# Kernel tuning notes

Hardware: AMD Instinct MI355X
Metric: run time of the kernel (lower is better)

## Reference

```python
import jax, jax.numpy as jnp
import numpy as np

EPS_N = 1e-12   # F.normalize eps
LN_EPS = 1e-5   # LayerNorm eps
N_NODES = 20000
NODES_PER_GRAPH = 200
DEG = 8
N_EDGES = N_NODES * DEG
F_NODE = 36
F_EDGE = 10
HID = 128
HEAD = 8
DK = HID // HEAD
G = N_NODES // NODES_PER_GRAPH


def l2norm(x):
    n = jnp.sqrt(jnp.sum(x * x, axis=-1, keepdims=True))
    return x / jnp.maximum(n, EPS_N)


def layer_norm(x, g, b):
    m = jnp.mean(x, axis=-1, keepdims=True)
    v = jnp.mean((x - m) ** 2, axis=-1, keepdims=True)
    return (x - m) / jnp.sqrt(v + LN_EPS) * g + b


def seg_softmax(e, idx, n):
    m = jax.ops.segment_max(e, idx, num_segments=n)
    ex = jnp.exp(e - m[idx])
    s = jax.ops.segment_sum(ex, idx, num_segments=n)
    return ex / s[idx]


def sfe_conv(x, src, dst, eattr, We, Wq, Wk, Wv, Wo, bo, g, b):
    # x: [N, in], src/dst: [Ef] (self loops included), eattr: [Ef, F_EDGE]
    n = x.shape[0]
    emb = l2norm(eattr @ We)                  # edge_encoder + F.normalize
    xj = x[src] + emb                          # source node + edge embedding
    q = (xj @ Wq).reshape(-1, HEAD, DK)
    ksum = (x[dst] @ Wk).reshape(-1, HEAD, DK).sum(axis=1)  # sum over k-heads (matmul+sum in source)
    v = (xj @ Wv).reshape(-1, HEAD, DK)
    energy = jnp.einsum('ehd,ed->eh', q, ksum) / jnp.sqrt(jnp.float32(HID))
    att = seg_softmax(energy, dst, n)          # segment softmax over target nodes, per head
    msg = (v * att[:, :, None]).reshape(-1, HID)
    agg = jax.ops.segment_sum(msg, dst, num_segments=n)
    y = layer_norm(agg @ Wo + bo, g, b)        # update(): out_norm(out_linear(.))
    return layer_norm(y, g, b)                 # forward() applies out_norm again


def setup_inputs():
    key = jax.random.key(0)
    ks = jax.random.split(key, 16)
    x = jax.random.normal(ks[0], (N_NODES, F_NODE), jnp.float32)
    edge_attr = jax.random.uniform(ks[1], (N_EDGES, F_EDGE), jnp.float32)
    src = jnp.repeat(jnp.arange(N_NODES), DEG)
    base = src - src % NODES_PER_GRAPH
    off = jax.random.randint(ks[2], (N_EDGES,), 1, NODES_PER_GRAPH)
    dst = base + (src % NODES_PER_GRAPH + off) % NODES_PER_GRAPH  # same-graph, no self loops
    edge_index = jnp.stack([src, dst]).astype(jnp.int64)
    batch = (jnp.arange(N_NODES) // NODES_PER_GRAPH).astype(jnp.int64)
    interface_pos = jnp.arange(0, N_NODES, 2, dtype=jnp.int64)
    s = lambda k, sh: jax.random.normal(k, sh, jnp.float32) * 0.05
    return dict(
        x=x, edge_attr=edge_attr,
        c0_We=s(ks[3], (F_EDGE, F_NODE)), c0_Wq=s(ks[4], (F_NODE, HID)),
        c0_Wk=s(ks[5], (F_NODE, HID)), c0_Wv=s(ks[6], (F_NODE, HID)),
        c0_Wo=s(ks[7], (HID, HID)), c0_bo=jnp.zeros((HID,), jnp.float32),
        c0_g=jnp.ones((HID,), jnp.float32), c0_b=jnp.zeros((HID,), jnp.float32),
        cs_We=s(ks[8], (2, F_EDGE, HID)), cs_Wq=s(ks[9], (2, HID, HID)),
        cs_Wk=s(ks[10], (2, HID, HID)), cs_Wv=s(ks[11], (2, HID, HID)),
        cs_Wo=s(ks[12], (2, HID, HID)), cs_bo=jnp.zeros((2, HID), jnp.float32),
        cs_g=jnp.ones((2, HID), jnp.float32), cs_b=jnp.zeros((2, HID), jnp.float32),
        gate=s(ks[13], (HID,)), W1=s(ks[14], (HID, HID // 2)),
        b1=jnp.zeros((HID // 2,), jnp.float32), W2=s(ks[15], (HID // 2, 1)),
        b2=jnp.zeros((1,), jnp.float32),
        edge_index=edge_index, batch=batch, interface_pos=interface_pos,
        graph_num=G)


def reference(x, edge_attr, c0_We, c0_Wq, c0_Wk, c0_Wv, c0_Wo, c0_bo, c0_g, c0_b,
              cs_We, cs_Wq, cs_Wk, cs_Wv, cs_Wo, cs_bo, cs_g, cs_b,
              gate, W1, b1, W2, b2, edge_index, batch, interface_pos, graph_num):
    n = x.shape[0]
    loops = jnp.arange(n)
    src = jnp.concatenate([edge_index[0], loops])
    dst = jnp.concatenate([edge_index[1], loops])
    ea = jnp.concatenate([l2norm(edge_attr),
                          jnp.zeros((n, edge_attr.shape[1]), edge_attr.dtype)])
    h = l2norm(x)
    h = jnp.tanh(sfe_conv(h, src, dst, ea, c0_We, c0_Wq, c0_Wk, c0_Wv, c0_Wo, c0_bo, c0_g, c0_b))
    for i in range(cs_We.shape[0]):
        h = jnp.tanh(sfe_conv(h, src, dst, ea, cs_We[i], cs_Wq[i], cs_Wk[i], cs_Wv[i],
                              cs_Wo[i], cs_bo[i], cs_g[i], cs_b[i]))
    # global self-attention pooling over interface nodes, per graph
    xi = h[interface_pos]
    bi = batch[interface_pos]
    att = seg_softmax(xi @ gate, bi, graph_num)
    pooled = jax.ops.segment_sum(att[:, None] * xi, bi, num_segments=graph_num)  # [G, HID]
    out = jnp.tanh(pooled @ W1 + b1)
    return jax.nn.sigmoid(out @ W2 + b2)  # [G, 1]
```

## Files before the change

### kernel.cpp

```cpp
#include <hip/hip_runtime.h>
#include <math.h>

#define HID 128
#define HEAD 8
#define DK 16
#define FEDGE 10
#define FNODE 36
#define ESCALE 0.08838834764831845f
#define CH 32

typedef float f32x4v __attribute__((ext_vector_type(4)));
typedef short bf16x8 __attribute__((ext_vector_type(8)));

struct PackArgs {
  const float* src[8];
  unsigned short* dst[8];
  int fin[8];
  int kt[8];
  int blk_off[8];
};

struct PrepArgs {
  const float* We[3];
  const float* Wq[3];
  const float* Wk[3];
  const float* Wv[3];
  float* C[3];
  float* WeWv[3];
  float* Gram[3];
  float* Wksum[3];
  int fin[3];
};

__device__ __forceinline__ void fma4(float4& z, float s, const float4& w) {
  z.x += s * w.x;
  z.y += s * w.y;
  z.z += s * w.z;
  z.w += s * w.w;
}

__device__ __forceinline__ unsigned short f2bf(float f) {
  unsigned int u = __float_as_uint(f);
  u += 0x7fffu + ((u >> 16) & 1u);
  return (unsigned short)(u >> 16);
}

__device__ __forceinline__ void store_bf8(unsigned short* p, float4 a, float4 b) {
  uint4 u;
  u.x = (unsigned)f2bf(a.x) | ((unsigned)f2bf(a.y) << 16);
  u.y = (unsigned)f2bf(a.z) | ((unsigned)f2bf(a.w) << 16);
  u.z = (unsigned)f2bf(b.x) | ((unsigned)f2bf(b.y) << 16);
  u.w = (unsigned)f2bf(b.z) | ((unsigned)f2bf(b.w) << 16);
  *(uint4*)p = u;
}

__global__ void k_zero_i(int* __restrict__ p, int n) {
  int i = blockIdx.x * 256 + threadIdx.x;
  if (i < n) p[i] = 0;
}

__global__ void k_count(const int* __restrict__ ei, int E, int* __restrict__ cnt) {
  int e = blockIdx.x * 256 + threadIdx.x;
  if (e >= E) return;
  atomicAdd(&cnt[ei[E + e]], 1);
}

__global__ __launch_bounds__(1024) void k_scan(const int* __restrict__ cnt, int* __restrict__ off,
                                               int* __restrict__ cur, int* __restrict__ scsr_s,
                                               int n, int total) {
  __shared__ int s[1024];
  int t = threadIdx.x;
  const int C = (n + 1023) / 1024;
  int local[32];
  int base = t * C;
  int sum = 0;
  for (int j = 0; j < C; ++j) {
    int i = base + j;
    int v = (i < n) ? cnt[i] : 0;
    local[j] = sum;
    sum += v;
  }
  s[t] = sum;
  __syncthreads();
  for (int dd = 1; dd < 1024; dd <<= 1) {
    int v = (t >= dd) ? s[t - dd] : 0;
    __syncthreads();
    s[t] += v;
    __syncthreads();
  }
  int excl = (t == 0) ? 0 : s[t - 1];
  for (int j = 0; j < C; ++j) {
    int i = base + j;
    if (i < n) {
      int o = excl + local[j];
      off[i] = o;
      cur[i] = o;
      scsr_s[o + i] = i;
    }
  }
  if (t == 0) off[n] = total;
}

__global__ void k_fill(const int* __restrict__ ei, int E, int* __restrict__ cur,
                       int* __restrict__ scsr_s, int* __restrict__ pmap) {
  int e = blockIdx.x * 256 + threadIdx.x;
  if (e >= E) return;
  int t = ei[E + e];
  int pos = atomicAdd(&cur[t], 1) + t + 1;
  pmap[e] = pos;
  scsr_s[pos] = ei[e];
}

__global__ __launch_bounds__(128) void k_wprep3(PrepArgs a) {
  int l = blockIdx.x / FEDGE, t = blockIdx.x - l * FEDGE;
  int d = threadIdx.x;
  int fin = a.fin[l];
  const float* We = a.We[l];
  const float* Wq = a.Wq[l];
  const float* Wk = a.Wk[l];
  const float* Wv = a.Wv[l];
  __shared__ float sw[HID];
  if (d < fin) sw[d] = We[t * fin + d];
  __syncthreads();
  float c = 0.f, wv = 0.f;
  for (int i = 0; i < fin; ++i) {
    c += sw[i] * Wq[i * HID + d];
    wv += sw[i] * Wv[i * HID + d];
  }
  a.C[l][t * HID + d] = c;
  a.WeWv[l][t * HID + d] = wv;
  if (d < FEDGE) {
    float g = 0.f;
    for (int i = 0; i < fin; ++i) g += sw[i] * We[d * fin + i];
    a.Gram[l][t * FEDGE + d] = g;
  }
  for (int r = t; r < fin; r += FEDGE) {
    if (d < DK) {
      float s = 0.f;
#pragma unroll
      for (int hh = 0; hh < HEAD; ++hh) s += Wk[r * HID + hh * DK + d];
      a.Wksum[l][r * DK + d] = s;
    }
  }
}

__global__ __launch_bounds__(64) void k_wpack8(PackArgs pa) {
  int b = blockIdx.x, lane = threadIdx.x;
  int m = 0;
#pragma unroll
  for (int i = 1; i < 8; ++i) m += (b >= pa.blk_off[i]);
  int local = b - pa.blk_off[m];
  int KT = pa.kt[m];
  int ct = local / KT, kt = local - ct * KT;
  const float* W = pa.src[m];
  int fin = pa.fin[m];
  int col = ct * 16 + (lane & 15);
  int kbase = kt * 32 + (lane >> 4) * 8;
  float v[8];
#pragma unroll
  for (int j = 0; j < 8; ++j) {
    int k = kbase + j;
    v[j] = (k < fin) ? W[k * HID + col] : 0.f;
  }
  store_bf8(pa.dst[m] + (size_t)local * 512 + lane * 8, make_float4(v[0], v[1], v[2], v[3]),
            make_float4(v[4], v[5], v[6], v[7]));
}

__global__ void k_l2e_sea(const float* __restrict__ eattr, const int* __restrict__ pmap,
                          const float* __restrict__ Gram3, float* __restrict__ sea3, int E,
                          int ET) {
  int e = blockIdx.x * 256 + threadIdx.x;
  if (e >= E) return;
  float a[FEDGE];
  float ss = 0.f;
  for (int i = 0; i < FEDGE; ++i) {
    a[i] = eattr[(size_t)e * FEDGE + i];
    ss += a[i] * a[i];
  }
  float s0 = 1.f / fmaxf(sqrtf(ss), 1e-12f);
  for (int i = 0; i < FEDGE; ++i) a[i] *= s0;
  int pos = pmap[e];
  for (int l = 0; l < 3; ++l) {
    const float* G = Gram3 + l * FEDGE * FEDGE;
    float gp = 0.f;
#pragma unroll
    for (int j = 0; j < FEDGE; ++j) {
      float t = 0.f;
#pragma unroll
      for (int u = 0; u < FEDGE; ++u) t += G[j * FEDGE + u] * a[u];
      gp += t * a[j];
    }
    float scl = 1.f / fmaxf(sqrtf(gp), 1e-12f);
    float* sp = sea3 + (size_t)l * ET * FEDGE + (size_t)pos * FEDGE;
#pragma unroll
    for (int u = 0; u < FEDGE; ++u) sp[u] = scl * a[u];
  }
}

__global__ __launch_bounds__(256) void k1_l2x(
    const float* __restrict__ x, const unsigned short* __restrict__ qpack,
    const unsigned short* __restrict__ vpack, const float* __restrict__ Wksum,
    const float* __restrict__ C, float* __restrict__ qx, float* __restrict__ kb,
    float* __restrict__ vxb, float* __restrict__ Mout, int N) {
  const int fin = FNODE;
  int d = threadIdx.x;
  int n0 = blockIdx.x * 16;
  int nb = min(16, N - n0);
  __shared__ __align__(16) float sx[16][40];
  __shared__ __align__(16) unsigned short afrag[2][64][8];
  __shared__ float sk[16][DK];
  {
    int col = d & 127, h2 = d >> 7;
#pragma unroll
    for (int rr = 0; rr < 8; ++rr) {
      int r = h2 * 8 + rr;
      if (col < fin) sx[r][col] = (r < nb) ? x[(size_t)(n0 + r) * fin + col] : 0.f;
    }
  }
  __syncthreads();
  int grp = d >> 4, j16 = d & 15;
  {
    float ssq = 0.f;
    for (int i = j16; i < fin; i += 16) ssq += sx[grp][i] * sx[grp][i];
#pragma unroll
    for (int o = 8; o; o >>= 1) ssq += __shfl_xor(ssq, o, 16);
    float scl = 1.f / fmaxf(sqrtf(ssq), 1e-12f);
    for (int i = j16; i < fin; i += 16) sx[grp][i] *= scl;
  }
  __syncthreads();
  int lane = d & 63, wvid = d >> 6;
  if (d < 128) {
    int kt = d >> 6;
    int m = lane & 15, k0 = kt * 32 + (lane >> 4) * 8;
    float v[8];
#pragma unroll
    for (int j = 0; j < 8; ++j) {
      int k = k0 + j;
      v[j] = (k < fin) ? sx[m][k] : 0.f;
    }
    store_bf8(&afrag[kt][lane][0], make_float4(v[0], v[1], v[2], v[3]),
              make_float4(v[4], v[5], v[6], v[7]));
  }
  {
    float kk = 0.f;
    for (int i = 0; i < fin; ++i) kk += sx[grp][i] * Wksum[i * DK + j16];
    sk[grp][j16] = kk;
    if (grp < nb) kb[(size_t)(n0 + grp) * DK + j16] = kk;
  }
  __syncthreads();
  int colD = lane & 15, quad = lane >> 4;
#pragma unroll
  for (int t = 0; t < 4; ++t) {
    int g = wvid * 4 + t;
    int mat = g >> 3, ct = g & 7;
    const unsigned short* P = mat ? vpack : qpack;
    f32x4v acc = {0.f, 0.f, 0.f, 0.f};
#pragma unroll
    for (int kt = 0; kt < 2; ++kt) {
      bf16x8 a = *(const bf16x8*)&afrag[kt][lane][0];
      bf16x8 b = *(const bf16x8*)(P + ((size_t)(ct * 2 + kt) * 64 + lane) * 8);
      acc = __builtin_amdgcn_mfma_f32_16x16x32_bf16(a, b, acc, 0, 0, 0);
    }
    float* out = mat ? vxb : qx;
#pragma unroll
    for (int reg = 0; reg < 4; ++reg) {
      int node = quad * 4 + reg;
      if (node < nb) out[(size_t)(n0 + node) * HID + ct * 16 + colD] = acc[reg];
    }
  }
  if (d < HEAD * FEDGE) {
    int hh = d / FEDGE, tt = d - hh * FEDGE;
    float crow[16];
    *(float4*)&crow[0] = *(const float4*)&C[tt * HID + hh * DK + 0];
    *(float4*)&crow[4] = *(const float4*)&C[tt * HID + hh * DK + 4];
    *(float4*)&crow[8] = *(const float4*)&C[tt * HID + hh * DK + 8];
    *(float4*)&crow[12] = *(const float4*)&C[tt * HID + hh * DK + 12];
    for (int r = 0; r < nb; ++r) {
      float m = 0.f;
#pragma unroll
      for (int j = 0; j < DK; ++j) m += sk[r][j] * crow[j];
      Mout[((size_t)(n0 + r) * HEAD + hh) * 16 + tt] = m;
    }
  }
}

__global__ __launch_bounds__(256) void k_post_k1(
    const float* __restrict__ agg, const unsigned short* __restrict__ opack,
    const float* __restrict__ bo, const float* __restrict__ gg, const float* __restrict__ bb,
    const unsigned short* __restrict__ qpack, const unsigned short* __restrict__ vpack,
    const float* __restrict__ Wksum, const float* __restrict__ C, float* __restrict__ qx,
    float* __restrict__ kb, float* __restrict__ vxb, float* __restrict__ Mout, int N) {
  int d = threadIdx.x;
  int n0 = blockIdx.x * 16;
  int nb = min(16, N - n0);
  __shared__ __align__(16) unsigned short afrag[4][64][8];
  __shared__ __align__(16) float sz[16][132];
  __shared__ __align__(16) unsigned short hfrag[4][64][8];
  __shared__ float sk[16][DK];
  int lane = d & 63, wvid = d >> 6;
  {
    int kt = wvid;
    int m = lane & 15, k0 = kt * 32 + (lane >> 4) * 8;
    const float* p = agg + (size_t)(n0 + m) * HID + k0;
    float4 x0 = *(const float4*)p;
    float4 x1 = *(const float4*)(p + 4);
    store_bf8(&afrag[kt][lane][0], x0, x1);
  }
  __syncthreads();
  int colD = lane & 15, quad = lane >> 4;
  {
    int ct0 = wvid * 2, ct1 = wvid * 2 + 1;
    float bias0 = bo[ct0 * 16 + colD], bias1 = bo[ct1 * 16 + colD];
    f32x4v acc0 = {bias0, bias0, bias0, bias0};
    f32x4v acc1 = {bias1, bias1, bias1, bias1};
#pragma unroll
    for (int kt = 0; kt < 4; ++kt) {
      bf16x8 a = *(const bf16x8*)&afrag[kt][lane][0];
      bf16x8 b0 = *(const bf16x8*)(opack + ((size_t)(ct0 * 4 + kt) * 64 + lane) * 8);
      bf16x8 b1 = *(const bf16x8*)(opack + ((size_t)(ct1 * 4 + kt) * 64 + lane) * 8);
      acc0 = __builtin_amdgcn_mfma_f32_16x16x32_bf16(a, b0, acc0, 0, 0, 0);
      acc1 = __builtin_amdgcn_mfma_f32_16x16x32_bf16(a, b1, acc1, 0, 0, 0);
    }
#pragma unroll
    for (int reg = 0; reg < 4; ++reg) {
      int node = quad * 4 + reg;
      sz[node][ct0 * 16 + colD] = acc0[reg];
      sz[node][ct1 * 16 + colD] = acc1[reg];
    }
  }
  __syncthreads();
  {
    int c4 = d & 31, rs = d >> 5;
    int col0 = c4 * 4, r0 = rs * 2;
    float4 zA = *(const float4*)&sz[r0][col0];
    float4 zB = *(const float4*)&sz[r0 + 1][col0];
    float4 g4 = *(const float4*)&gg[col0];
    float4 b4 = *(const float4*)&bb[col0];
#pragma unroll
    for (int pass = 0; pass < 2; ++pass) {
      float sA = zA.x + zA.y + zA.z + zA.w;
      float qA = zA.x * zA.x + zA.y * zA.y + zA.z * zA.z + zA.w * zA.w;
      float sB = zB.x + zB.y + zB.z + zB.w;
      float qB = zB.x * zB.x + zB.y * zB.y + zB.z * zB.z + zB.w * zB.w;
#pragma unroll
      for (int o = 16; o; o >>= 1) {
        sA += __shfl_xor(sA, o, 32);
        qA += __shfl_xor(qA, o, 32);
        sB += __shfl_xor(sB, o, 32);
        qB += __shfl_xor(qB, o, 32);
      }
      float mA = sA * (1.f / 128.f);
      float iA = rsqrtf(fmaxf(qA * (1.f / 128.f) - mA * mA, 0.f) + 1e-5f);
      float mB = sB * (1.f / 128.f);
      float iB = rsqrtf(fmaxf(qB * (1.f / 128.f) - mB * mB, 0.f) + 1e-5f);
      zA.x = (zA.x - mA) * iA * g4.x + b4.x;
      zA.y = (zA.y - mA) * iA * g4.y + b4.y;
      zA.z = (zA.z - mA) * iA * g4.z + b4.z;
      zA.w = (zA.w - mA) * iA * g4.w + b4.w;
      zB.x = (zB.x - mB) * iB * g4.x + b4.x;
      zB.y = (zB.y - mB) * iB * g4.y + b4.y;
      zB.z = (zB.z - mB) * iB * g4.z + b4.z;
      zB.w = (zB.w - mB) * iB * g4.w + b4.w;
    }
    zA.x = tanhf(zA.x);
    zA.y = tanhf(zA.y);
    zA.z = tanhf(zA.z);
    zA.w = tanhf(zA.w);
    zB.x = tanhf(zB.x);
    zB.y = tanhf(zB.y);
    zB.z = tanhf(zB.z);
    zB.w = tanhf(zB.w);
    *(float4*)&sz[r0][col0] = zA;
    *(float4*)&sz[r0 + 1][col0] = zB;
    int chunk = col0 >> 5, qd = (col0 >> 3) & 3, eo = col0 & 7;
    unsigned int loA = (unsigned)f2bf(zA.x) | ((unsigned)f2bf(zA.y) << 16);
    unsigned int hiA = (unsigned)f2bf(zA.z) | ((unsigned)f2bf(zA.w) << 16);
    unsigned int loB = (unsigned)f2bf(zB.x) | ((unsigned)f2bf(zB.y) << 16);
    unsigned int hiB = (unsigned)f2bf(zB.z) | ((unsigned)f2bf(zB.w) << 16);
    unsigned short* pA = &hfrag[chunk][(r0 & 15) + qd * 16][eo];
    unsigned short* pB = &hfrag[chunk][((r0 + 1) & 15) + qd * 16][eo];
    *(unsigned int*)pA = loA;
    *(unsigned int*)(pA + 2) = hiA;
    *(unsigned int*)pB = loB;
    *(unsigned int*)(pB + 2) = hiB;
  }
  __syncthreads();
#pragma unroll
  for (int t = 0; t < 4; ++t) {
    int g = wvid * 4 + t;
    int mat = g >> 3, ct = g & 7;
    const unsigned short* P = mat ? vpack : qpack;
    f32x4v acc = {0.f, 0.f, 0.f, 0.f};
#pragma unroll
    for (int kt = 0; kt < 4; ++kt) {
      bf16x8 a = *(const bf16x8*)&hfrag[kt][lane][0];
      bf16x8 b = *(const bf16x8*)(P + ((size_t)(ct * 4 + kt) * 64 + lane) * 8);
      acc = __builtin_amdgcn_mfma_f32_16x16x32_bf16(a, b, acc, 0, 0, 0);
    }
    float* out = mat ? vxb : qx;
#pragma unroll
    for (int reg = 0; reg < 4; ++reg) {
      int node = quad * 4 + reg;
      if (node < nb) out[(size_t)(n0 + node) * HID + ct * 16 + colD] = acc[reg];
    }
  }
  int grp = d >> 4, j16 = d & 15;
  {
    float kk = 0.f;
    for (int i = 0; i < HID; ++i) kk += sz[grp][i] * Wksum[i * DK + j16];
    sk[grp][j16] = kk;
    if (grp < nb) kb[(size_t)(n0 + grp) * DK + j16] = kk;
  }
  __syncthreads();
  if (d < HEAD * FEDGE) {
    int hh = d / FEDGE, tt = d - hh * FEDGE;
    float crow[16];
    *(float4*)&crow[0] = *(const float4*)&C[tt * HID + hh * DK + 0];
    *(float4*)&crow[4] = *(const float4*)&C[tt * HID + hh * DK + 4];
    *(float4*)&crow[8] = *(const float4*)&C[tt * HID + hh * DK + 8];
    *(float4*)&crow[12] = *(const float4*)&C[tt * HID + hh * DK + 12];
    for (int r = 0; r < nb; ++r) {
      float m = 0.f;
#pragma unroll
      for (int j = 0; j < DK; ++j) m += sk[r][j] * crow[j];
      Mout[((size_t)(n0 + r) * HEAD + hh) * 16 + tt] = m;
    }
  }
}

__global__ __launch_bounds__(128) void k3_gather(
    const int* __restrict__ off, const int* __restrict__ scsr_s, const float* __restrict__ sea,
    const float* __restrict__ qx, const float* __restrict__ kb, const float* __restrict__ Mbuf,
    const float* __restrict__ vxb, const float* __restrict__ WeWv, float* __restrict__ agg,
    int N) {
  int b = blockIdx.x;
  int n = ((N & 7) == 0) ? ((b & 7) * (N >> 3) + (b >> 3)) : b;
  int d = threadIdx.x;
  int j16 = d & 15, hd = d >> 4;
  __shared__ float sen[CH * 8];
  __shared__ float ssea[CH * 10];
  __shared__ int ss[CH];
  __shared__ float sT[HEAD * FEDGE];
  __shared__ __align__(16) float skb[DK];
  __shared__ float sM[128];
  int base = off[n] + n;
  int cnt = off[n + 1] + n + 1 - base;
  if (d < DK) skb[d] = kb[(size_t)n * DK + d];
  sM[d] = Mbuf[(size_t)n * 128 + d];
  bool doT = (j16 < FEDGE);
  float m = -1e30f, l = 0.f, accv = 0.f, T = 0.f;
  for (int c0 = 0; c0 < cnt; c0 += CH) {
    int cc = min(CH, cnt - c0);
    for (int idx = d; idx < cc * 10; idx += 128)
      ssea[idx] = sea[(size_t)(base + c0) * 10 + idx];
    if (d < cc) ss[d] = scsr_s[base + c0 + d];
    __syncthreads();
    for (int ob = 0; ob < cc; ob += 16) {
      int o = ob + (d >> 3);
      int h = d & 7;
      if (o < cc) {
        int s = ss[o];
        const float4* qp = (const float4*)(qx + (size_t)s * HID + h * DK);
        float en = 0.f;
#pragma unroll
        for (int j4 = 0; j4 < 4; ++j4) {
          float4 q4 = qp[j4];
          float4 k4 = *(const float4*)&skb[j4 * 4];
          en += q4.x * k4.x + q4.y * k4.y + q4.z * k4.z + q4.w * k4.w;
        }
        if ((c0 + o) > 0) {
#pragma unroll
          for (int u = 0; u < FEDGE; ++u) en += sM[h * DK + u] * ssea[o * 10 + u];
        }
        sen[o * 8 + h] = en * ESCALE;
      }
    }
    __syncthreads();
    float mloc = -1e30f;
    for (int o = 0; o < cc; ++o) mloc = fmaxf(mloc, sen[o * 8 + hd]);
    float mnew = fmaxf(m, mloc);
    float alpha = __expf(m - mnew);
    l *= alpha;
    accv *= alpha;
    T *= alpha;
#pragma unroll 2
    for (int o = 0; o < cc; ++o) {
      int s = ss[o];
      float p = __expf(sen[o * 8 + hd] - mnew);
      l += p;
      accv += p * vxb[(size_t)s * HID + d];
      if (doT && (c0 + o) > 0) T += p * ssea[o * 10 + j16];
    }
    m = mnew;
    __syncthreads();
  }
  float inv = 1.f / l;
  if (doT) sT[hd * FEDGE + j16] = T * inv;
  __syncthreads();
  float y = accv * inv;
#pragma unroll
  for (int t = 0; t < FEDGE; ++t) y += sT[hd * FEDGE + t] * WeWv[t * HID + d];
  agg[(size_t)n * HID + d] = y;
}

__global__ __launch_bounds__(256) void k_post(const float* __restrict__ agg,
                                              const float* __restrict__ Wo,
                                              const float* __restrict__ bo,
                                              const float* __restrict__ gg,
                                              const float* __restrict__ bb,
                                              float* __restrict__ hout, int N) {
  int d = threadIdx.x;
  int n0 = blockIdx.x * 16;
  int nb = min(16, N - n0);
  __shared__ __align__(16) float sh[16][132];
  {
    int col = d & 127, h2 = d >> 7;
#pragma unroll
    for (int rr = 0; rr < 8; ++rr) {
      int r = h2 * 8 + rr;
      sh[r][col] = (r < nb) ? agg[(size_t)(n0 + r) * HID + col] : 0.f;
    }
  }
  __syncthreads();
  int c4 = d & 31, rs = d >> 5;
  int col0 = c4 * 4, r0 = rs * 2;
  float4 bv = *(const float4*)&bo[col0];
  float4 zA = bv, zB = bv;
  for (int k4 = 0; k4 < 32; ++k4) {
    float4 w0 = *(const float4*)&Wo[(k4 * 4 + 0) * HID + col0];
    float4 w1 = *(const float4*)&Wo[(k4 * 4 + 1) * HID + col0];
    float4 w2 = *(const float4*)&Wo[(k4 * 4 + 2) * HID + col0];
    float4 w3 = *(const float4*)&Wo[(k4 * 4 + 3) * HID + col0];
    float4 a0 = *(const float4*)&sh[r0][k4 * 4];
    float4 a1 = *(const float4*)&sh[r0 + 1][k4 * 4];
    fma4(zA, a0.x, w0);
    fma4(zA, a0.y, w1);
    fma4(zA, a0.z, w2);
    fma4(zA, a0.w, w3);
    fma4(zB, a1.x, w0);
    fma4(zB, a1.y, w1);
    fma4(zB, a1.z, w2);
    fma4(zB, a1.w, w3);
  }
  float4 g4 = *(const float4*)&gg[col0];
  float4 b4 = *(const float4*)&bb[col0];
#pragma unroll
  for (int pass = 0; pass < 2; ++pass) {
    float sA = zA.x + zA.y + zA.z + zA.w;
    float qA = zA.x * zA.x + zA.y * zA.y + zA.z * zA.z + zA.w * zA.w;
    float sB = zB.x + zB.y + zB.z + zB.w;
    float qB = zB.x * zB.x + zB.y * zB.y + zB.z * zB.z + zB.w * zB.w;
#pragma unroll
    for (int o = 16; o; o >>= 1) {
      sA += __shfl_xor(sA, o, 32);
      qA += __shfl_xor(qA, o, 32);
      sB += __shfl_xor(sB, o, 32);
      qB += __shfl_xor(qB, o, 32);
    }
    float mA = sA * (1.f / 128.f);
    float iA = rsqrtf(fmaxf(qA * (1.f / 128.f) - mA * mA, 0.f) + 1e-5f);
    float mB = sB * (1.f / 128.f);
    float iB = rsqrtf(fmaxf(qB * (1.f / 128.f) - mB * mB, 0.f) + 1e-5f);
    zA.x = (zA.x - mA) * iA * g4.x + b4.x;
    zA.y = (zA.y - mA) * iA * g4.y + b4.y;
    zA.z = (zA.z - mA) * iA * g4.z + b4.z;
    zA.w = (zA.w - mA) * iA * g4.w + b4.w;
    zB.x = (zB.x - mB) * iB * g4.x + b4.x;
    zB.y = (zB.y - mB) * iB * g4.y + b4.y;
    zB.z = (zB.z - mB) * iB * g4.z + b4.z;
    zB.w = (zB.w - mB) * iB * g4.w + b4.w;
  }
  if (r0 < nb) {
    float4 o0 = make_float4(tanhf(zA.x), tanhf(zA.y), tanhf(zA.z), tanhf(zA.w));
    *(float4*)&hout[(size_t)(n0 + r0) * HID + col0] = o0;
  }
  if (r0 + 1 < nb) {
    float4 o1 = make_float4(tanhf(zB.x), tanhf(zB.y), tanhf(zB.z), tanhf(zB.w));
    *(float4*)&hout[(size_t)(n0 + r0 + 1) * HID + col0] = o1;
  }
}

__global__ __launch_bounds__(128) void k4_pool(const float* __restrict__ h,
                                               const int* __restrict__ ipos,
                                               const float* __restrict__ gate,
                                               const float* __restrict__ W1,
                                               const float* __restrict__ b1,
                                               const float* __restrict__ W2,
                                               const float* __restrict__ b2,
                                               float* __restrict__ out, int per_g) {
  int g = blockIdx.x, d = threadIdx.x;
  __shared__ int snode[128];
  __shared__ float satt[128], spool[HID], so[64], sv[2];
  if (d < per_g) snode[d] = ipos[g * per_g + d];
  __syncthreads();
  float sc = -1e30f;
  if (d < per_g) {
    float s = 0.f;
    int node = snode[d];
    for (int i = 0; i < HID; ++i) s += h[(size_t)node * HID + i] * gate[i];
    sc = s;
  }
  satt[d] = sc;
  __syncthreads();
  if (d == 0) {
    float m = -1e30f;
    for (int i = 0; i < per_g; ++i) m = fmaxf(m, satt[i]);
    sv[0] = m;
  }
  __syncthreads();
  float m = sv[0];
  float ex = (d < per_g) ? __expf(sc - m) : 0.f;
  satt[d] = ex;
  __syncthreads();
  if (d == 0) {
    float su = 0.f;
    for (int i = 0; i < per_g; ++i) su += satt[i];
    sv[1] = 1.f / su;
  }
  __syncthreads();
  float inv = sv[1];
  float p = 0.f;
  for (int i = 0; i < per_g; ++i) p += satt[i] * h[(size_t)snode[i] * HID + d];
  spool[d] = p * inv;
  __syncthreads();
  if (d < 64) {
    float o = b1[d];
    for (int i = 0; i < HID; ++i) o += spool[i] * W1[i * 64 + d];
    so[d] = tanhf(o);
  }
  __syncthreads();
  if (d == 0) {
    float z = b2[0];
    for (int i = 0; i < 64; ++i) z += so[i] * W2[i];
    out[g] = 1.f / (1.f + __expf(-z));
  }
}

extern "C" void kernel_launch(void* const* d_in, const int* in_sizes, int n_in, void* d_out,
                              int out_size, void* d_ws, size_t ws_size, hipStream_t stream) {
  const float* x = (const float*)d_in[0];
  const float* eattr = (const float*)d_in[1];
  const float* c0_We = (const float*)d_in[2];
  const float* c0_Wq = (const float*)d_in[3];
  const float* c0_Wk = (const float*)d_in[4];
  const float* c0_Wv = (const float*)d_in[5];
  const float* c0_Wo = (const float*)d_in[6];
  const float* c0_bo = (const float*)d_in[7];
  const float* c0_g = (const float*)d_in[8];
  const float* c0_b = (const float*)d_in[9];
  const float* cs_We = (const float*)d_in[10];
  const float* cs_Wq = (const float*)d_in[11];
  const float* cs_Wk = (const float*)d_in[12];
  const float* cs_Wv = (const float*)d_in[13];
  const float* cs_Wo = (const float*)d_in[14];
  const float* cs_bo = (const float*)d_in[15];
  const float* cs_g = (const float*)d_in[16];
  const float* cs_b = (const float*)d_in[17];
  const float* gate = (const float*)d_in[18];
  const float* W1 = (const float*)d_in[19];
  const float* b1 = (const float*)d_in[20];
  const float* W2 = (const float*)d_in[21];
  const float* b2 = (const float*)d_in[22];
  const int* ei = (const int*)d_in[23];
  const int* ipos = (const int*)d_in[25];

  int N = in_sizes[0] / FNODE;
  int E = in_sizes[1] / FEDGE;
  int G = out_size;
  int per_g = in_sizes[25] / G;
  int ET = E + N;

  float* w = (float*)d_ws;
  float* hB = w;         w += (size_t)N * HID;
  float* qx = w;         w += (size_t)N * HID;
  float* aggb = w;       w += (size_t)N * HID;
  float* kb = w;         w += (size_t)N * DK;
  float* vx = w;         w += (size_t)N * HID;
  float* Mbuf = w;       w += (size_t)N * HEAD * 16;
  float* sea3 = w;       w += (size_t)3 * ET * FEDGE;
  float* C3 = w;         w += 3 * FEDGE * HID;
  float* WeWv3 = w;      w += 3 * FEDGE * HID;
  float* Gram3 = w;      w += 3 * FEDGE * FEDGE;
  float* Wksum3 = w;     w += 3 * HID * DK;
  unsigned short* qp3 = (unsigned short*)w;  w += 3 * 16384 / 2;
  unsigned short* vp3 = (unsigned short*)w;  w += 3 * 16384 / 2;
  unsigned short* op2 = (unsigned short*)w;  w += 2 * 16384 / 2;
  int* cnt = (int*)w;
  int* off = cnt + (N + 1);
  int* cur = off + (N + 1);
  int* scsr_s = cur + N;
  int* pmap = scsr_s + ET;

  const float* Ws[3][8] = {
      {c0_We, c0_Wq, c0_Wk, c0_Wv, c0_Wo, c0_bo, c0_g, c0_b},
      {cs_We, cs_Wq, cs_Wk, cs_Wv, cs_Wo, cs_bo, cs_g, cs_b},
      {cs_We + FEDGE * HID, cs_Wq + HID * HID, cs_Wk + HID * HID, cs_Wv + HID * HID,
       cs_Wo + HID * HID, cs_bo + HID, cs_g + HID, cs_b + HID}};
  int fins[3] = {FNODE, HID, HID};

  PrepArgs prep;
  for (int l = 0; l < 3; ++l) {
    prep.We[l] = Ws[l][0];
    prep.Wq[l] = Ws[l][1];
    prep.Wk[l] = Ws[l][2];
    prep.Wv[l] = Ws[l][3];
    prep.C[l] = C3 + l * FEDGE * HID;
    prep.WeWv[l] = WeWv3 + l * FEDGE * HID;
    prep.Gram[l] = Gram3 + l * FEDGE * FEDGE;
    prep.Wksum[l] = Wksum3 + l * HID * DK;
    prep.fin[l] = fins[l];
  }
  k_wprep3<<<3 * FEDGE, 128, 0, stream>>>(prep);

  PackArgs pa;
  {
    const float* srcs[8] = {Ws[0][1], Ws[0][3], Ws[1][1], Ws[1][3],
                            Ws[2][1], Ws[2][3], Ws[0][4], Ws[1][4]};
    unsigned short* dsts[8] = {qp3, vp3, qp3 + 16384, vp3 + 16384, qp3 + 2 * 16384,
                               vp3 + 2 * 16384, op2, op2 + 16384};
    int fns[8] = {FNODE, FNODE, HID, HID, HID, HID, HID, HID};
    int kts[8] = {2, 2, 4, 4, 4, 4, 4, 4};
    int offb = 0;
    for (int i = 0; i < 8; ++i) {
      pa.src[i] = srcs[i];
      pa.dst[i] = dsts[i];
      pa.fin[i] = fns[i];
      pa.kt[i] = kts[i];
      pa.blk_off[i] = offb;
      offb += 8 * kts[i];
    }
    k_wpack8<<<offb, 64, 0, stream>>>(pa);
  }

  k_zero_i<<<(N + 1 + 255) / 256, 256, 0, stream>>>(cnt, N + 1);
  k_count<<<(E + 255) / 256, 256, 0, stream>>>(ei, E, cnt);
  k_scan<<<1, 1024, 0, stream>>>(cnt, off, cur, scsr_s, N, E);
  k_fill<<<(E + 255) / 256, 256, 0, stream>>>(ei, E, cur, scsr_s, pmap);
  k_l2e_sea<<<(E + 255) / 256, 256, 0, stream>>>(eattr, pmap, Gram3, sea3, E, ET);

  k1_l2x<<<(N + 15) / 16, 256, 0, stream>>>(x, qp3, vp3, Wksum3, C3, qx, kb, vx, Mbuf, N);
  for (int l = 0; l < 3; ++l) {
    const float* sea_l = sea3 + (size_t)l * ET * FEDGE;
    k3_gather<<<N, 128, 0, stream>>>(off, scsr_s, sea_l, qx, kb, Mbuf, vx,
                                     WeWv3 + l * FEDGE * HID, aggb, N);
    if (l < 2) {
      k_post_k1<<<(N + 15) / 16, 256, 0, stream>>>(
          aggb, op2 + l * 16384, Ws[l][5], Ws[l][6], Ws[l][7], qp3 + (l + 1) * 16384,
          vp3 + (l + 1) * 16384, Wksum3 + (l + 1) * HID * DK, C3 + (l + 1) * FEDGE * HID, qx, kb,
          vx, Mbuf, N);
    } else {
      k_post<<<(N + 15) / 16, 256, 0, stream>>>(aggb, Ws[l][4], Ws[l][5], Ws[l][6], Ws[l][7], hB,
                                                N);
    }
  }
  k4_pool<<<G, 128, 0, stream>>>(hB, ipos, gate, W1, b1, W2, b2, (float*)d_out, per_g);
}
```

Before: 403.5 us.

## Store q/v projections in bf16 and fuse edge fill with edge-attr scaling

The per-node q and v projections are now written as bf16 instead of fp32, and the gather kernel unpacks them on load. This halves the bytes read in the edge-gather stage, which is random-access and memory bound. Separately, the CSR fill kernel is merged with the edge-attribute normalisation kernel, removing one launch and the pmap intermediate buffer. Storing bf16 activations adds rounding error to the attention energies and messages.

```diff
diff --git a/kernel.cpp b/kernel.cpp
--- a/kernel.cpp
+++ b/kernel.cpp
@@ -44,6 +44,9 @@
   u += 0x7fffu + ((u >> 16) & 1u);
   return (unsigned short)(u >> 16);
 }
+
+__device__ __forceinline__ float bflo(unsigned int u) { return __uint_as_float(u << 16); }
+__device__ __forceinline__ float bfhi(unsigned int u) { return __uint_as_float(u & 0xffff0000u); }
 
 __device__ __forceinline__ void store_bf8(unsigned short* p, float4 a, float4 b) {
   uint4 u;
@@ -101,14 +104,37 @@
   if (t == 0) off[n] = total;
 }
 
-__global__ void k_fill(const int* __restrict__ ei, int E, int* __restrict__ cur,
-                       int* __restrict__ scsr_s, int* __restrict__ pmap) {
+__global__ void k_fill_sea(const int* __restrict__ ei, int E, int* __restrict__ cur,
+                           int* __restrict__ scsr_s, const float* __restrict__ eattr,
+                           const float* __restrict__ Gram3, float* __restrict__ sea3, int ET) {
   int e = blockIdx.x * 256 + threadIdx.x;
   if (e >= E) return;
   int t = ei[E + e];
   int pos = atomicAdd(&cur[t], 1) + t + 1;
-  pmap[e] = pos;
   scsr_s[pos] = ei[e];
+  float a[FEDGE];
+  float ss = 0.f;
+  for (int i = 0; i < FEDGE; ++i) {
+    a[i] = eattr[(size_t)e * FEDGE + i];
+    ss += a[i] * a[i];
+  }
+  float s0 = 1.f / fmaxf(sqrtf(ss), 1e-12f);
+  for (int i = 0; i < FEDGE; ++i) a[i] *= s0;
+  for (int l = 0; l < 3; ++l) {
+    const float* G = Gram3 + l * FEDGE * FEDGE;
+    float gp = 0.f;
+#pragma unroll
+    for (int j = 0; j < FEDGE; ++j) {
+      float tt = 0.f;
+#pragma unroll
+      for (int u = 0; u < FEDGE; ++u) tt += G[j * FEDGE + u] * a[u];
+      gp += tt * a[j];
+    }
+    float scl = 1.f / fmaxf(sqrtf(gp), 1e-12f);
+    float* sp = sea3 + (size_t)l * ET * FEDGE + (size_t)pos * FEDGE;
+#pragma unroll
+    for (int u = 0; u < FEDGE; ++u) sp[u] = scl * a[u];
+  }
 }
 
 __global__ __launch_bounds__(128) void k_wprep3(PrepArgs a) {
@@ -166,42 +192,11 @@
             make_float4(v[4], v[5], v[6], v[7]));
 }
 
-__global__ void k_l2e_sea(const float* __restrict__ eattr, const int* __restrict__ pmap,
-                          const float* __restrict__ Gram3, float* __restrict__ sea3, int E,
-                          int ET) {
-  int e = blockIdx.x * 256 + threadIdx.x;
-  if (e >= E) return;
-  float a[FEDGE];
-  float ss = 0.f;
-  for (int i = 0; i < FEDGE; ++i) {
-    a[i] = eattr[(size_t)e * FEDGE + i];
-    ss += a[i] * a[i];
-  }
-  float s0 = 1.f / fmaxf(sqrtf(ss), 1e-12f);
-  for (int i = 0; i < FEDGE; ++i) a[i] *= s0;
-  int pos = pmap[e];
-  for (int l = 0; l < 3; ++l) {
-    const float* G = Gram3 + l * FEDGE * FEDGE;
-    float gp = 0.f;
-#pragma unroll
-    for (int j = 0; j < FEDGE; ++j) {
-      float t = 0.f;
-#pragma unroll
-      for (int u = 0; u < FEDGE; ++u) t += G[j * FEDGE + u] * a[u];
-      gp += t * a[j];
-    }
-    float scl = 1.f / fmaxf(sqrtf(gp), 1e-12f);
-    float* sp = sea3 + (size_t)l * ET * FEDGE + (size_t)pos * FEDGE;
-#pragma unroll
-    for (int u = 0; u < FEDGE; ++u) sp[u] = scl * a[u];
-  }
-}
-
 __global__ __launch_bounds__(256) void k1_l2x(
     const float* __restrict__ x, const unsigned short* __restrict__ qpack,
     const unsigned short* __restrict__ vpack, const float* __restrict__ Wksum,
-    const float* __restrict__ C, float* __restrict__ qx, float* __restrict__ kb,
-    float* __restrict__ vxb, float* __restrict__ Mout, int N) {
+    const float* __restrict__ C, unsigned short* __restrict__ qxh, float* __restrict__ kb,
+    unsigned short* __restrict__ vxh, float* __restrict__ Mout, int N) {
   const int fin = FNODE;
   int d = threadIdx.x;
   int n0 = blockIdx.x * 16;
@@ -261,11 +256,11 @@
       bf16x8 b = *(const bf16x8*)(P + ((size_t)(ct * 2 + kt) * 64 + lane) * 8);
       acc = __builtin_amdgcn_mfma_f32_16x16x32_bf16(a, b, acc, 0, 0, 0);
     }
-    float* out = mat ? vxb : qx;
+    unsigned short* out = mat ? vxh : qxh;
 #pragma unroll
     for (int reg = 0; reg < 4; ++reg) {
       int node = quad * 4 + reg;
-      if (node < nb) out[(size_t)(n0 + node) * HID + ct * 16 + colD] = acc[reg];
+      if (node < nb) out[(size_t)(n0 + node) * HID + ct * 16 + colD] = f2bf(acc[reg]);
     }
   }
   if (d < HEAD * FEDGE) {
@@ -288,8 +283,9 @@
     const float* __restrict__ agg, const unsigned short* __restrict__ opack,
     const float* __restrict__ bo, const float* __restrict__ gg, const float* __restrict__ bb,
     const unsigned short* __restrict__ qpack, const unsigned short* __restrict__ vpack,
-    const float* __restrict__ Wksum, const float* __restrict__ C, float* __restrict__ qx,
-    float* __restrict__ kb, float* __restrict__ vxb, float* __restrict__ Mout, int N) {
+    const float* __restrict__ Wksum, const float* __restrict__ C,
+    unsigned short* __restrict__ qxh, float* __restrict__ kb, unsigned short* __restrict__ vxh,
+    float* __restrict__ Mout, int N) {
   int d = threadIdx.x;
   int n0 = blockIdx.x * 16;
   int nb = min(16, N - n0);
@@ -397,11 +393,11 @@
       bf16x8 b = *(const bf16x8*)(P + ((size_t)(ct * 4 + kt) * 64 + lane) * 8);
       acc = __builtin_amdgcn_mfma_f32_16x16x32_bf16(a, b, acc, 0, 0, 0);
     }
-    float* out = mat ? vxb : qx;
+    unsigned short* out = mat ? vxh : qxh;
 #pragma unroll
     for (int reg = 0; reg < 4; ++reg) {
       int node = quad * 4 + reg;
-      if (node < nb) out[(size_t)(n0 + node) * HID + ct * 16 + colD] = acc[reg];
+      if (node < nb) out[(size_t)(n0 + node) * HID + ct * 16 + colD] = f2bf(acc[reg]);
     }
   }
   int grp = d >> 4, j16 = d & 15;
@@ -430,9 +426,9 @@
 
 __global__ __launch_bounds__(128) void k3_gather(
     const int* __restrict__ off, const int* __restrict__ scsr_s, const float* __restrict__ sea,
-    const float* __restrict__ qx, const float* __restrict__ kb, const float* __restrict__ Mbuf,
-    const float* __restrict__ vxb, const float* __restrict__ WeWv, float* __restrict__ agg,
-    int N) {
+    const unsigned short* __restrict__ qxh, const float* __restrict__ kb,
+    const float* __restrict__ Mbuf, const unsigned short* __restrict__ vxh,
+    const float* __restrict__ WeWv, float* __restrict__ agg, int N) {
   int b = blockIdx.x;
   int n = ((N & 7) == 0) ? ((b & 7) * (N >> 3) + (b >> 3)) : b;
   int d = threadIdx.x;
@@ -460,14 +456,14 @@
       int h = d & 7;
       if (o < cc) {
         int s = ss[o];
-        const float4* qp = (const float4*)(qx + (size_t)s * HID + h * DK);
-        float en = 0.f;
-#pragma unroll
-        for (int j4 = 0; j4 < 4; ++j4) {
-          float4 q4 = qp[j4];
-          float4 k4 = *(const float4*)&skb[j4 * 4];
-          en += q4.x * k4.x + q4.y * k4.y + q4.z * k4.z + q4.w * k4.w;
-        }
+        const uint4* qp = (const uint4*)(qxh + (size_t)s * HID + h * DK);
+        uint4 qa = qp[0], qb = qp[1];
+        float en = bflo(qa.x) * skb[0] + bfhi(qa.x) * skb[1] + bflo(qa.y) * skb[2] +
+                   bfhi(qa.y) * skb[3] + bflo(qa.z) * skb[4] + bfhi(qa.z) * skb[5] +
+                   bflo(qa.w) * skb[6] + bfhi(qa.w) * skb[7] + bflo(qb.x) * skb[8] +
+                   bfhi(qb.x) * skb[9] + bflo(qb.y) * skb[10] + bfhi(qb.y) * skb[11] +
+                   bflo(qb.z) * skb[12] + bfhi(qb.z) * skb[13] + bflo(qb.w) * skb[14] +
+                   bfhi(qb.w) * skb[15];
         if ((c0 + o) > 0) {
 #pragma unroll
           for (int u = 0; u < FEDGE; ++u) en += sM[h * DK + u] * ssea[o * 10 + u];
@@ -488,7 +484,8 @@
       int s = ss[o];
       float p = __expf(sen[o * 8 + hd] - mnew);
       l += p;
-      accv += p * vxb[(size_t)s * HID + d];
+      float vv = __uint_as_float((unsigned)vxh[(size_t)s * HID + d] << 16);
+      accv += p * vv;
       if (doT && (c0 + o) > 0) T += p * ssea[o * 10 + j16];
     }
     m = mnew;
@@ -672,16 +669,16 @@
 
   float* w = (float*)d_ws;
   float* hB = w;         w += (size_t)N * HID;
-  float* qx = w;         w += (size_t)N * HID;
   float* aggb = w;       w += (size_t)N * HID;
   float* kb = w;         w += (size_t)N * DK;
-  float* vx = w;         w += (size_t)N * HID;
   float* Mbuf = w;       w += (size_t)N * HEAD * 16;
   float* sea3 = w;       w += (size_t)3 * ET * FEDGE;
   float* C3 = w;         w += 3 * FEDGE * HID;
   float* WeWv3 = w;      w += 3 * FEDGE * HID;
   float* Gram3 = w;      w += 3 * FEDGE * FEDGE;
   float* Wksum3 = w;     w += 3 * HID * DK;
+  unsigned short* qxh = (unsigned short*)w;  w += (size_t)N * HID / 2;
+  unsigned short* vxh = (unsigned short*)w;  w += (size_t)N * HID / 2;
   unsigned short* qp3 = (unsigned short*)w;  w += 3 * 16384 / 2;
   unsigned short* vp3 = (unsigned short*)w;  w += 3 * 16384 / 2;
   unsigned short* op2 = (unsigned short*)w;  w += 2 * 16384 / 2;
@@ -689,7 +686,6 @@
   int* off = cnt + (N + 1);
   int* cur = off + (N + 1);
   int* scsr_s = cur + N;
-  int* pmap = scsr_s + ET;
 
   const float* Ws[3][8] = {
       {c0_We, c0_Wq, c0_Wk, c0_Wv, c0_Wo, c0_bo, c0_g, c0_b},
@@ -735,19 +731,18 @@
   k_zero_i<<<(N + 1 + 255) / 256, 256, 0, stream>>>(cnt, N + 1);
   k_count<<<(E + 255) / 256, 256, 0, stream>>>(ei, E, cnt);
   k_scan<<<1, 1024, 0, stream>>>(cnt, off, cur, scsr_s, N, E);
-  k_fill<<<(E + 255) / 256, 256, 0, stream>>>(ei, E, cur, scsr_s, pmap);
-  k_l2e_sea<<<(E + 255) / 256, 256, 0, stream>>>(eattr, pmap, Gram3, sea3, E, ET);
-
-  k1_l2x<<<(N + 15) / 16, 256, 0, stream>>>(x, qp3, vp3, Wksum3, C3, qx, kb, vx, Mbuf, N);
+  k_fill_sea<<<(E + 255) / 256, 256, 0, stream>>>(ei, E, cur, scsr_s, eattr, Gram3, sea3, ET);
+
+  k1_l2x<<<(N + 15) / 16, 256, 0, stream>>>(x, qp3, vp3, Wksum3, C3, qxh, kb, vxh, Mbuf, N);
   for (int l = 0; l < 3; ++l) {
     const float* sea_l = sea3 + (size_t)l * ET * FEDGE;
-    k3_gather<<<N, 128, 0, stream>>>(off, scsr_s, sea_l, qx, kb, Mbuf, vx,
+    k3_gather<<<N, 128, 0, stream>>>(off, scsr_s, sea_l, qxh, kb, Mbuf, vxh,
                                      WeWv3 + l * FEDGE * HID, aggb, N);
     if (l < 2) {
       k_post_k1<<<(N + 15) / 16, 256, 0, stream>>>(
           aggb, op2 + l * 16384, Ws[l][5], Ws[l][6], Ws[l][7], qp3 + (l + 1) * 16384,
-          vp3 + (l + 1) * 16384, Wksum3 + (l + 1) * HID * DK, C3 + (l + 1) * FEDGE * HID, qx, kb,
-          vx, Mbuf, N);
+          vp3 + (l + 1) * 16384, Wksum3 + (l + 1) * HID * DK, C3 + (l + 1) * FEDGE * HID, qxh, kb,
+          vxh, Mbuf, N);
     } else {
       k_post<<<(N + 15) / 16, 256, 0, stream>>>(aggb, Ws[l][4], Ws[l][5], Ws[l][6], Ws[l][7], hB,
                                                 N);
```

Measured after the change: 392.0 us. 1.03x faster.
